# Kernel optimization log

Hardware: AMD Instinct MI355X
Metric: run time of the kernel (lower is better)

## Reference

```python
import jax, jax.numpy as jnp
import numpy as np

ENC_DIM, DEC_DIM, HID_DIM = 512, 1024, 128
B, T = 64, 2048


def setup_inputs() -> dict:
    key = jax.random.key(0)
    ks = jax.random.split(key, 8)
    encoder_outs = jax.random.normal(ks[0], (B, T, ENC_DIM), dtype=jnp.float32)
    decoder_state = jax.random.normal(ks[1], (B, DEC_DIM), dtype=jnp.float32)
    mask = jax.random.randint(ks[2], (B, T), 0, 2) == 1
    # parameters (torch nn.Linear: y = x @ W.T + b)
    sV = 1.0 / np.sqrt(ENC_DIM)
    sW = 1.0 / np.sqrt(DEC_DIM)
    sw = 1.0 / np.sqrt(HID_DIM)
    V_w = jax.random.uniform(ks[3], (HID_DIM, ENC_DIM), minval=-sV, maxval=sV)
    V_b = jax.random.uniform(ks[4], (HID_DIM,), minval=-sV, maxval=sV)
    W_w = jax.random.uniform(ks[5], (HID_DIM, DEC_DIM), minval=-sW, maxval=sW)
    w_w = jax.random.uniform(ks[6], (1, HID_DIM), minval=-sw, maxval=sw)
    w_b = jax.random.uniform(ks[7], (1,), minval=-sw, maxval=sw)
    return {"encoder_outs": encoder_outs, "decoder_state": decoder_state,
            "mask": mask, "V_w": V_w, "V_b": V_b, "W_w": W_w,
            "w_w": w_w, "w_b": w_b}


def reference(encoder_outs, decoder_state, mask, V_w, V_b, W_w, w_w, w_b):
    # [B,1,H] query projection + [B,T,H] key projection
    q = jnp.einsum('bd,hd->bh', decoder_state, W_w)[:, None, :]
    k = jnp.einsum('bte,he->bth', encoder_outs, V_w) + V_b
    # scores: [B,T]
    erg = jnp.einsum('bth,h->bt', jnp.tanh(q + k), w_w[0]) + w_b[0]
    erg = jnp.where(mask, -jnp.inf, erg)
    attention_weights = jax.nn.softmax(erg, axis=1)
    attention_context = jnp.einsum('bte,bt->be', encoder_outs, attention_weights)
    return (attention_context, attention_weights)
```

## Files before the change

### kernel.cpp

```cpp
#include <hip/hip_runtime.h>
#include <hip/hip_bf16.h>

#define Bn   64
#define Tn   2048
#define ENCD 512
#define DECD 1024
#define HIDD 128
#define TT   32
#define NCH  (Tn / TT)
#define LROW 520

typedef __attribute__((ext_vector_type(8))) short bf16x8;
typedef __attribute__((ext_vector_type(4))) float f32x4;

__device__ __forceinline__ unsigned short f2bf(float f) {
    union { float f; unsigned u; } v; v.f = f;
    unsigned r = v.u + 0x7FFFu + ((v.u >> 16) & 1u);
    return (unsigned short)(r >> 16);
}
__device__ __forceinline__ float bf2f(unsigned short s) {
    union { unsigned u; float f; } v; v.u = ((unsigned)s) << 16;
    return v.f;
}
__device__ __forceinline__ float tanh_fast(float x) {
    float xa = fminf(fmaxf(x, -10.f), 10.f);
    float e = __expf(2.f * xa);
    return (e - 1.f) / (e + 1.f);
}

__global__ __launch_bounds__(256) void prep(
    const float* __restrict__ dec, const float* __restrict__ Ww,
    const float* __restrict__ Vb,  const float* __restrict__ Vw,
    float* __restrict__ qb, unsigned short* __restrict__ Vbf)
{
    const int blk = blockIdx.x, tid = threadIdx.x;
    if (blk < 512) {
        const int b = blk >> 3, hg = blk & 7;
        const int h_local = tid >> 4, seg = tid & 15;
        const int h = hg * 16 + h_local;
        const float4* w = (const float4*)(Ww + (size_t)h * DECD);
        const float4* d = (const float4*)(dec + (size_t)b * DECD);
        float acc = 0.f;
        #pragma unroll
        for (int j = 0; j < 16; ++j) {
            int f4 = j * 16 + seg;
            float4 a = d[f4], bb = w[f4];
            acc += a.x * bb.x + a.y * bb.y + a.z * bb.z + a.w * bb.w;
        }
        acc += __shfl_xor(acc, 1);
        acc += __shfl_xor(acc, 2);
        acc += __shfl_xor(acc, 4);
        acc += __shfl_xor(acc, 8);
        if (seg == 0) qb[b * HIDD + h] = acc + Vb[h];
    } else {
        const int c = blk - 512;
        const float4* src = (const float4*)Vw;
        #pragma unroll
        for (int i = 0; i < 2; ++i) {
            int f4 = c * 512 + tid * 2 + i;
            float4 v = src[f4];
            ushort4 u;
            u.x = f2bf(v.x); u.y = f2bf(v.y); u.z = f2bf(v.z); u.w = f2bf(v.w);
            *(ushort4*)&Vbf[f4 * 4] = u;
        }
    }
}

__global__ __launch_bounds__(512, 8) void attn_main(
    const float* __restrict__ enc, const int* __restrict__ mask,
    const float* __restrict__ qb,  const unsigned short* __restrict__ Vbf,
    const float* __restrict__ ww,  const float* __restrict__ wb,
    float* __restrict__ pW, float* __restrict__ mC, float* __restrict__ lC,
    float* __restrict__ ctxP)
{
    __shared__ unsigned short encS[TT * LROW];
    __shared__ float wpart[8][TT];
    __shared__ float pS[TT];

    const int chunk = blockIdx.x, b = blockIdx.y;
    const int tid = threadIdx.x;
    const int t0 = chunk * TT;
    const int wave = tid >> 6, lane = tid & 63;
    const int li = lane & 15, quad = lane >> 4;

    const int h = wave * 16 + li;
    const float qv = qb[b * HIDD + h];
    const float wv = ww[h];

    const float* encTile = enc + ((size_t)b * Tn + t0) * ENCD;
    {
        float4 v[8];
        #pragma unroll
        for (int it = 0; it < 8; ++it)
            v[it] = ((const float4*)encTile)[it * 512 + tid];
        #pragma unroll
        for (int it = 0; it < 8; ++it) {
            int f4 = it * 512 + tid;
            int t = f4 >> 7, e = (f4 & 127) * 4;
            ushort4 u;
            u.x = f2bf(v[it].x); u.y = f2bf(v[it].y);
            u.z = f2bf(v[it].z); u.w = f2bf(v[it].w);
            *(ushort4*)&encS[t * LROW + e] = u;
        }
    }
    __syncthreads();

    f32x4 acc[2];
    acc[0] = (f32x4){0.f, 0.f, 0.f, 0.f};
    acc[1] = (f32x4){0.f, 0.f, 0.f, 0.f};
    const unsigned short* vrow = Vbf + (size_t)h * ENCD;

    #pragma unroll 4
    for (int ks = 0; ks < 16; ++ks) {
        int k0 = ks * 32 + quad * 8;
        bf16x8 a0 = *(const bf16x8*)&encS[(0  + li) * LROW + k0];
        bf16x8 a1 = *(const bf16x8*)&encS[(16 + li) * LROW + k0];
        bf16x8 bb = *(const bf16x8*)(vrow + k0);
        acc[0] = __builtin_amdgcn_mfma_f32_16x16x32_bf16(a0, bb, acc[0], 0, 0, 0);
        acc[1] = __builtin_amdgcn_mfma_f32_16x16x32_bf16(a1, bb, acc[1], 0, 0, 0);
    }

    #pragma unroll
    for (int mt = 0; mt < 2; ++mt)
        #pragma unroll
        for (int r = 0; r < 4; ++r) {
            float s = tanh_fast(acc[mt][r] + qv) * wv;
            s += __shfl_xor(s, 1);
            s += __shfl_xor(s, 2);
            s += __shfl_xor(s, 4);
            s += __shfl_xor(s, 8);
            if (li == 0) wpart[wave][mt * 16 + quad * 4 + r] = s;
        }
    __syncthreads();

    if (wave == 0) {
        float e = -INFINITY;
        if (lane < TT) {
            int t = lane;
            float v = wb[0];
            #pragma unroll
            for (int w = 0; w < 8; ++w) v += wpart[w][t];
            e = (mask[b * Tn + t0 + t] != 0) ? -INFINITY : v;
        }
        float m = e;
        #pragma unroll
        for (int off = 32; off >= 1; off >>= 1)
            m = fmaxf(m, __shfl_xor(m, off));
        float p = (e == -INFINITY) ? 0.f : __expf(e - m);
        float l = p;
        #pragma unroll
        for (int off = 32; off >= 1; off >>= 1)
            l += __shfl_xor(l, off);
        if (lane < TT) {
            pS[lane] = p;
            pW[(size_t)b * Tn + t0 + lane] = p;
        }
        if (lane == 0) {
            mC[b * NCH + chunk] = m;
            lC[b * NCH + chunk] = l;
        }
    }
    __syncthreads();

    {
        float c = 0.f;
        #pragma unroll 8
        for (int t = 0; t < TT; ++t)
            c += pS[t] * bf2f(encS[t * LROW + tid]);
        ctxP[((size_t)(b * NCH + chunk)) * ENCD + tid] = c;
    }
}

__global__ __launch_bounds__(256) void finalize(
    const float* __restrict__ mC, const float* __restrict__ lC,
    const float* __restrict__ pW, const float* __restrict__ ctxP,
    float* __restrict__ out)
{
    __shared__ float scaleS[NCH];
    __shared__ float invLs;
    __shared__ float red[256];
    const int b = blockIdx.x, part = blockIdx.y, tid = threadIdx.x;
    const int wave = tid >> 6, lane = tid & 63;

    if (wave == 0) {
        float m = mC[b * NCH + lane];
        float l = lC[b * NCH + lane];
        float gm = m;
        #pragma unroll
        for (int off = 32; off >= 1; off >>= 1)
            gm = fmaxf(gm, __shfl_xor(gm, off));
        float sc = (m == -INFINITY) ? 0.f : __expf(m - gm);
        float ls = l * sc;
        #pragma unroll
        for (int off = 32; off >= 1; off >>= 1)
            ls += __shfl_xor(ls, off);
        scaleS[lane] = sc;
        if (lane == 0) invLs = 1.f / ls;
    }
    __syncthreads();
    const float invL = invLs;

    if (part < 4) {
        const int e = part * 128 + (tid & 127);
        const int half = tid >> 7;
        float c = 0.f;
        #pragma unroll 8
        for (int cc = half * 32; cc < half * 32 + 32; ++cc)
            c += scaleS[cc] * ctxP[((size_t)(b * NCH + cc)) * ENCD + e];
        red[tid] = c;
        __syncthreads();
        if (tid < 128) {
            int ee = part * 128 + tid;
            out[b * ENCD + ee] = (red[tid] + red[tid + 128]) * invL;
        }
    } else {
        float* outw = out + Bn * ENCD;
        #pragma unroll
        for (int i = 0; i < 8; ++i) {
            int t = i * 256 + tid;
            outw[(size_t)b * Tn + t] = pW[(size_t)b * Tn + t] * scaleS[t >> 5] * invL;
        }
    }
}

extern "C" void kernel_launch(void* const* d_in, const int* in_sizes, int n_in,
                              void* d_out, int out_size, void* d_ws, size_t ws_size,
                              hipStream_t stream)
{
    const float* enc  = (const float*)d_in[0];
    const float* dec  = (const float*)d_in[1];
    const int*   mask = (const int*)d_in[2];
    const float* Vw   = (const float*)d_in[3];
    const float* Vb   = (const float*)d_in[4];
    const float* Ww   = (const float*)d_in[5];
    const float* ww   = (const float*)d_in[6];
    const float* wb   = (const float*)d_in[7];
    float* out = (float*)d_out;
    float* ws  = (float*)d_ws;

    float*          qb   = ws;
    unsigned short* Vbf  = (unsigned short*)(ws + 8192);
    float*          pW   = ws + 40960;
    float*          mC   = ws + 172032;
    float*          lC   = ws + 176128;
    float*          ctxP = ws + 180224;

    hipLaunchKernelGGL(prep, dim3(576), dim3(256), 0, stream, dec, Ww, Vb, Vw, qb, Vbf);
    hipLaunchKernelGGL(attn_main, dim3(NCH, Bn), dim3(512), 0, stream,
                       enc, mask, qb, Vbf, ww, wb, pW, mC, lC, ctxP);
    hipLaunchKernelGGL(finalize, dim3(Bn, 5), dim3(256), 0, stream, mC, lC, pW, ctxP, out);
}
```

Measured before the change: 389.5 us.

## Process eight chunks per block with double-buffered encoder tiles and online softmax merge

Each attention block now walks eight consecutive 32-row chunks. While the MFMA scoring runs on the current tile, the next tile is loaded into registers, and it is written into a second LDS buffer afterwards. The per-chunk context partials are combined inside the block with an online-softmax rescale, so only one partial per group goes to global memory, and the finalize kernel becomes a single pass. The prep kernel's V weight conversion is also corrected to cover exactly the weight matrix. The trade-off is a grid of only 512 blocks with doubled LDS per block, which lowers occupancy and parallelism for this memory-bound stream.

```diff
diff --git a/kernel.cpp b/kernel.cpp
--- a/kernel.cpp
+++ b/kernel.cpp
@@ -1,5 +1,4 @@
 #include <hip/hip_runtime.h>
-#include <hip/hip_bf16.h>
 
 #define Bn   64
 #define Tn   2048
@@ -8,6 +7,8 @@
 #define HIDD 128
 #define TT   32
 #define NCH  (Tn / TT)
+#define CPG  8
+#define NGR  (NCH / CPG)
 #define LROW 520
 
 typedef __attribute__((ext_vector_type(8))) short bf16x8;
@@ -55,169 +56,198 @@
     } else {
         const int c = blk - 512;
         const float4* src = (const float4*)Vw;
-        #pragma unroll
-        for (int i = 0; i < 2; ++i) {
-            int f4 = c * 512 + tid * 2 + i;
-            float4 v = src[f4];
-            ushort4 u;
-            u.x = f2bf(v.x); u.y = f2bf(v.y); u.z = f2bf(v.z); u.w = f2bf(v.w);
-            *(ushort4*)&Vbf[f4 * 4] = u;
-        }
-    }
-}
-
-__global__ __launch_bounds__(512, 8) void attn_main(
+        int f4 = c * 256 + tid;
+        float4 v = src[f4];
+        ushort4 u;
+        u.x = f2bf(v.x); u.y = f2bf(v.y); u.z = f2bf(v.z); u.w = f2bf(v.w);
+        *(ushort4*)&Vbf[f4 * 4] = u;
+    }
+}
+
+__global__ __launch_bounds__(512, 4) void attn_main(
     const float* __restrict__ enc, const int* __restrict__ mask,
     const float* __restrict__ qb,  const unsigned short* __restrict__ Vbf,
     const float* __restrict__ ww,  const float* __restrict__ wb,
     float* __restrict__ pW, float* __restrict__ mC, float* __restrict__ lC,
-    float* __restrict__ ctxP)
-{
-    __shared__ unsigned short encS[TT * LROW];
+    float* __restrict__ ctxG, float* __restrict__ gmG)
+{
+    __shared__ unsigned short encS[2 * TT * LROW];
     __shared__ float wpart[8][TT];
     __shared__ float pS[TT];
-
-    const int chunk = blockIdx.x, b = blockIdx.y;
+    __shared__ float mS;
+
+    const int cg = blockIdx.x, b = blockIdx.y;
     const int tid = threadIdx.x;
-    const int t0 = chunk * TT;
     const int wave = tid >> 6, lane = tid & 63;
     const int li = lane & 15, quad = lane >> 4;
 
     const int h = wave * 16 + li;
     const float qv = qb[b * HIDD + h];
     const float wv = ww[h];
-
-    const float* encTile = enc + ((size_t)b * Tn + t0) * ENCD;
-    {
-        float4 v[8];
-        #pragma unroll
-        for (int it = 0; it < 8; ++it)
-            v[it] = ((const float4*)encTile)[it * 512 + tid];
-        #pragma unroll
-        for (int it = 0; it < 8; ++it) {
-            int f4 = it * 512 + tid;
-            int t = f4 >> 7, e = (f4 & 127) * 4;
-            ushort4 u;
-            u.x = f2bf(v[it].x); u.y = f2bf(v[it].y);
-            u.z = f2bf(v[it].z); u.w = f2bf(v[it].w);
-            *(ushort4*)&encS[t * LROW + e] = u;
-        }
+    const unsigned short* vrow = Vbf + (size_t)h * ENCD;
+
+    const float4* encBase =
+        (const float4*)(enc + ((size_t)b * Tn + (size_t)cg * (CPG * TT)) * ENCD);
+
+    float4 v[8];
+    #pragma unroll
+    for (int it = 0; it < 8; ++it) v[it] = encBase[it * 512 + tid];
+    #pragma unroll
+    for (int it = 0; it < 8; ++it) {
+        int f4 = it * 512 + tid;
+        int t = f4 >> 7, e2 = (f4 & 127) * 4;
+        ushort4 u;
+        u.x = f2bf(v[it].x); u.y = f2bf(v[it].y);
+        u.z = f2bf(v[it].z); u.w = f2bf(v[it].w);
+        *(ushort4*)&encS[t * LROW + e2] = u;
     }
     __syncthreads();
 
-    f32x4 acc[2];
-    acc[0] = (f32x4){0.f, 0.f, 0.f, 0.f};
-    acc[1] = (f32x4){0.f, 0.f, 0.f, 0.f};
-    const unsigned short* vrow = Vbf + (size_t)h * ENCD;
-
-    #pragma unroll 4
-    for (int ks = 0; ks < 16; ++ks) {
-        int k0 = ks * 32 + quad * 8;
-        bf16x8 a0 = *(const bf16x8*)&encS[(0  + li) * LROW + k0];
-        bf16x8 a1 = *(const bf16x8*)&encS[(16 + li) * LROW + k0];
-        bf16x8 bb = *(const bf16x8*)(vrow + k0);
-        acc[0] = __builtin_amdgcn_mfma_f32_16x16x32_bf16(a0, bb, acc[0], 0, 0, 0);
-        acc[1] = __builtin_amdgcn_mfma_f32_16x16x32_bf16(a1, bb, acc[1], 0, 0, 0);
-    }
-
-    #pragma unroll
-    for (int mt = 0; mt < 2; ++mt)
-        #pragma unroll
-        for (int r = 0; r < 4; ++r) {
-            float s = tanh_fast(acc[mt][r] + qv) * wv;
-            s += __shfl_xor(s, 1);
-            s += __shfl_xor(s, 2);
-            s += __shfl_xor(s, 4);
-            s += __shfl_xor(s, 8);
-            if (li == 0) wpart[wave][mt * 16 + quad * 4 + r] = s;
-        }
-    __syncthreads();
-
-    if (wave == 0) {
-        float e = -INFINITY;
-        if (lane < TT) {
-            int t = lane;
-            float v = wb[0];
-            #pragma unroll
-            for (int w = 0; w < 8; ++w) v += wpart[w][t];
-            e = (mask[b * Tn + t0 + t] != 0) ? -INFINITY : v;
-        }
-        float m = e;
-        #pragma unroll
-        for (int off = 32; off >= 1; off >>= 1)
-            m = fmaxf(m, __shfl_xor(m, off));
-        float p = (e == -INFINITY) ? 0.f : __expf(e - m);
-        float l = p;
-        #pragma unroll
-        for (int off = 32; off >= 1; off >>= 1)
-            l += __shfl_xor(l, off);
-        if (lane < TT) {
-            pS[lane] = p;
-            pW[(size_t)b * Tn + t0 + lane] = p;
-        }
-        if (lane == 0) {
-            mC[b * NCH + chunk] = m;
-            lC[b * NCH + chunk] = l;
-        }
-    }
-    __syncthreads();
-
-    {
-        float c = 0.f;
-        #pragma unroll 8
-        for (int t = 0; t < TT; ++t)
-            c += pS[t] * bf2f(encS[t * LROW + tid]);
-        ctxP[((size_t)(b * NCH + chunk)) * ENCD + tid] = c;
-    }
-}
-
-__global__ __launch_bounds__(256) void finalize(
+    float ctx = 0.f;
+    float gm  = -INFINITY;
+
+    for (int i = 0; i < CPG; ++i) {
+        unsigned short* sb = encS + (i & 1) * (TT * LROW);
+        const int chunk = cg * CPG + i;
+
+        f32x4 acc[2];
+        acc[0] = (f32x4){0.f, 0.f, 0.f, 0.f};
+        acc[1] = (f32x4){0.f, 0.f, 0.f, 0.f};
+        #pragma unroll 4
+        for (int ks = 0; ks < 16; ++ks) {
+            int k0 = ks * 32 + quad * 8;
+            bf16x8 a0 = *(const bf16x8*)&sb[(0  + li) * LROW + k0];
+            bf16x8 a1 = *(const bf16x8*)&sb[(16 + li) * LROW + k0];
+            bf16x8 bb = *(const bf16x8*)(vrow + k0);
+            acc[0] = __builtin_amdgcn_mfma_f32_16x16x32_bf16(a0, bb, acc[0], 0, 0, 0);
+            acc[1] = __builtin_amdgcn_mfma_f32_16x16x32_bf16(a1, bb, acc[1], 0, 0, 0);
+        }
+
+        if (i + 1 < CPG) {
+            #pragma unroll
+            for (int it = 0; it < 8; ++it)
+                v[it] = encBase[(i + 1) * (TT * ENCD / 4) + it * 512 + tid];
+        }
+
+        #pragma unroll
+        for (int mt = 0; mt < 2; ++mt)
+            #pragma unroll
+            for (int r = 0; r < 4; ++r) {
+                float s = tanh_fast(acc[mt][r] + qv) * wv;
+                s += __shfl_xor(s, 1);
+                s += __shfl_xor(s, 2);
+                s += __shfl_xor(s, 4);
+                s += __shfl_xor(s, 8);
+                if (li == 0) wpart[wave][mt * 16 + quad * 4 + r] = s;
+            }
+        __syncthreads();
+
+        if (wave == 0) {
+            float e = -INFINITY;
+            if (lane < TT) {
+                float vs = wb[0];
+                #pragma unroll
+                for (int w = 0; w < 8; ++w) vs += wpart[w][lane];
+                e = (mask[b * Tn + chunk * TT + lane] != 0) ? -INFINITY : vs;
+            }
+            float m = e;
+            #pragma unroll
+            for (int off = 32; off >= 1; off >>= 1)
+                m = fmaxf(m, __shfl_xor(m, off));
+            float p = (e == -INFINITY) ? 0.f : __expf(e - m);
+            float l = p;
+            #pragma unroll
+            for (int off = 32; off >= 1; off >>= 1)
+                l += __shfl_xor(l, off);
+            if (lane < TT) {
+                pS[lane] = p;
+                pW[(size_t)b * Tn + chunk * TT + lane] = p;
+            }
+            if (lane == 0) {
+                mC[b * NCH + chunk] = m;
+                lC[b * NCH + chunk] = l;
+                mS = m;
+            }
+        }
+        __syncthreads();
+
+        {
+            const float m = mS;
+            float sumt = 0.f;
+            #pragma unroll
+            for (int t = 0; t < TT; ++t)
+                sumt += pS[t] * bf2f(sb[t * LROW + tid]);
+            float nm = fmaxf(gm, m);
+            if (nm > -INFINITY) {
+                float rs = (gm > -INFINITY) ? __expf(gm - nm) : 0.f;
+                float as = (m  > -INFINITY) ? __expf(m  - nm) : 0.f;
+                ctx = ctx * rs + sumt * as;
+                gm = nm;
+            }
+        }
+
+        if (i + 1 < CPG) {
+            unsigned short* nb = encS + ((i + 1) & 1) * (TT * LROW);
+            #pragma unroll
+            for (int it = 0; it < 8; ++it) {
+                int f4 = it * 512 + tid;
+                int t = f4 >> 7, e2 = (f4 & 127) * 4;
+                ushort4 u;
+                u.x = f2bf(v[it].x); u.y = f2bf(v[it].y);
+                u.z = f2bf(v[it].z); u.w = f2bf(v[it].w);
+                *(ushort4*)&nb[t * LROW + e2] = u;
+            }
+        }
+        __syncthreads();
+    }
+
+    ctxG[((size_t)(b * NGR + cg)) * ENCD + tid] = ctx;
+    if (tid == 0) gmG[b * NGR + cg] = gm;
+}
+
+__global__ __launch_bounds__(512) void finalize(
     const float* __restrict__ mC, const float* __restrict__ lC,
-    const float* __restrict__ pW, const float* __restrict__ ctxP,
-    float* __restrict__ out)
+    const float* __restrict__ pW, const float* __restrict__ ctxG,
+    const float* __restrict__ gmG, float* __restrict__ out)
 {
     __shared__ float scaleS[NCH];
-    __shared__ float invLs;
-    __shared__ float red[256];
+    __shared__ float invLs, GMs;
     const int b = blockIdx.x, part = blockIdx.y, tid = threadIdx.x;
     const int wave = tid >> 6, lane = tid & 63;
 
     if (wave == 0) {
         float m = mC[b * NCH + lane];
         float l = lC[b * NCH + lane];
-        float gm = m;
+        float gmax = m;
         #pragma unroll
         for (int off = 32; off >= 1; off >>= 1)
-            gm = fmaxf(gm, __shfl_xor(gm, off));
-        float sc = (m == -INFINITY) ? 0.f : __expf(m - gm);
+            gmax = fmaxf(gmax, __shfl_xor(gmax, off));
+        float sc = (m == -INFINITY) ? 0.f : __expf(m - gmax);
         float ls = l * sc;
         #pragma unroll
         for (int off = 32; off >= 1; off >>= 1)
             ls += __shfl_xor(ls, off);
         scaleS[lane] = sc;
-        if (lane == 0) invLs = 1.f / ls;
+        if (lane == 0) { invLs = 1.f / ls; GMs = gmax; }
     }
     __syncthreads();
     const float invL = invLs;
 
-    if (part < 4) {
-        const int e = part * 128 + (tid & 127);
-        const int half = tid >> 7;
+    if (part == 0) {
+        const float GM = GMs;
         float c = 0.f;
-        #pragma unroll 8
-        for (int cc = half * 32; cc < half * 32 + 32; ++cc)
-            c += scaleS[cc] * ctxP[((size_t)(b * NCH + cc)) * ENCD + e];
-        red[tid] = c;
-        __syncthreads();
-        if (tid < 128) {
-            int ee = part * 128 + tid;
-            out[b * ENCD + ee] = (red[tid] + red[tid + 128]) * invL;
-        }
+        #pragma unroll
+        for (int g = 0; g < NGR; ++g) {
+            float gmv = gmG[b * NGR + g];
+            float gs = (gmv == -INFINITY) ? 0.f : __expf(gmv - GM);
+            c += gs * ctxG[((size_t)(b * NGR + g)) * ENCD + tid];
+        }
+        out[b * ENCD + tid] = c * invL;
     } else {
         float* outw = out + Bn * ENCD;
         #pragma unroll
-        for (int i = 0; i < 8; ++i) {
-            int t = i * 256 + tid;
+        for (int i = 0; i < 4; ++i) {
+            int t = i * 512 + tid;
             outw[(size_t)b * Tn + t] = pW[(size_t)b * Tn + t] * scaleS[t >> 5] * invL;
         }
     }
@@ -243,10 +273,11 @@
     float*          pW   = ws + 40960;
     float*          mC   = ws + 172032;
     float*          lC   = ws + 176128;
-    float*          ctxP = ws + 180224;
+    float*          ctxG = ws + 180224;
+    float*          gmG  = ws + 442368;
 
     hipLaunchKernelGGL(prep, dim3(576), dim3(256), 0, stream, dec, Ww, Vb, Vw, qb, Vbf);
-    hipLaunchKernelGGL(attn_main, dim3(NCH, Bn), dim3(512), 0, stream,
-                       enc, mask, qb, Vbf, ww, wb, pW, mC, lC, ctxP);
-    hipLaunchKernelGGL(finalize, dim3(Bn, 5), dim3(256), 0, stream, mC, lC, pW, ctxP, out);
-}
+    hipLaunchKernelGGL(attn_main, dim3(NGR, Bn), dim3(512), 0, stream,
+                       enc, mask, qb, Vbf, ww, wb, pW, mC, lC, ctxG, gmG);
+    hipLaunchKernelGGL(finalize, dim3(Bn, 2), dim3(512), 0, stream, mC, lC, pW, ctxG, gmG, out);
+}
```

Measured after the change: 398.6 us. 1.02x slower.
